# Optimization experiments

Measured on AMD Instinct MI355X. Metric: run time of the kernel, lower is better.

The kernel has to match this reference:

```python
import jax, jax.numpy as jnp
import numpy as np

H, U = 64, 64  # matrix-completion patch size; system size is (H*U)^2 = 4096^2


def svtC(X, tau):
    # Singular value thresholding: soft-threshold singular values by tau.
    u, s, vt = jnp.linalg.svd(X, full_matrices=False)
    return (u * jax.nn.relu(s - tau)) @ vt


def setup_inputs() -> dict:
    key = jax.random.key(0)
    ks = jax.random.split(key, 12)
    x = jax.random.normal(ks[0], (H, U), jnp.float32)
    L = jax.random.normal(ks[1], (H, U), jnp.float32)
    entries_mask = jax.random.randint(ks[2], (H, U), 0, 2).astype(bool)
    # D_tilda: symmetric PSD (HU, HU) smoothness operator so the system is well-conditioned
    M = jax.random.normal(ks[3], (H * U, H * U), jnp.float32)
    D_tilda = (M @ M.T) / jnp.float32(H * U)
    th_P = jax.random.normal(ks[4], (H, U), jnp.float32)
    v = jax.random.normal(ks[5], (), jnp.float32)
    coef_gamma = jax.random.uniform(ks[6], (), jnp.float32)
    neta = jax.random.uniform(ks[7], (), jnp.float32)
    lamda1 = jax.random.uniform(ks[8], (), jnp.float32)
    lamda2 = jax.random.uniform(ks[9], (), jnp.float32)
    rho = jax.random.uniform(ks[10], (), jnp.float32) + jnp.float32(0.1)
    S = jax.random.normal(ks[11], (H, H), jnp.float32) / np.float32(np.sqrt(H))
    return {"x": x, "L": L, "entries_mask": entries_mask, "D_tilda": D_tilda,
            "th_P": th_P, "v": v, "coef_gamma": coef_gamma, "neta": neta,
            "lamda1": lamda1, "lamda2": lamda2, "rho": rho, "S": S}


def reference(x, L, entries_mask, D_tilda, th_P, v, coef_gamma, neta,
              lamda1, lamda2, rho, S):
    tau = jax.nn.sigmoid(v) * coef_gamma
    # Q_tilda = diag(vec(mask)); S_tilda = kron(I_U, S^T S)
    q = entries_mask.astype(jnp.float32).reshape(-1)  # (HU,)
    StS = S.T @ S                                      # (H, H)
    S_tilda = jnp.kron(jnp.eye(U, dtype=jnp.float32), StS)  # (HU, HU)
    eye = jnp.eye(H * U, dtype=jnp.float32)
    A = jnp.diag(q) + lamda1 * D_tilda + lamda2 * S_tilda + rho * eye
    vec = rho * (L - th_P) + jnp.where(entries_mask, x, jnp.float32(0.0))
    # Original uses explicit dense inverse followed by matvec
    Xtmp = (jnp.linalg.inv(A) @ vec.reshape(-1)).reshape(H, U)
    Ltmp = svtC(Xtmp + th_P, tau)
    Ptmp = th_P + neta * (Xtmp - Ltmp)
    return Ltmp, Ptmp
```

## Files before the change

kernel.cpp:

```cpp
#include <hip/hip_runtime.h>
#include <cstddef>

#define HU    4096
#define NBLK  256
#define NTHR  512
#define MAXIT 100
#define TOL2  1e-7f

#define WS_STS  0
#define WS_DINV 4096
#define WS_R0   8192
#define WS_U0   12288
#define WS_W    16384
#define WS_BAR  24576
#define WS_FLG  (WS_BAR + 1024)
#define WS_END  (WS_FLG + 128)

typedef _Float16 half4v __attribute__((ext_vector_type(4)));

__device__ __forceinline__ float fastrcp(float x) {
  float r; asm("v_rcp_f32 %0, %1" : "=v"(r) : "v"(x)); return r;
}
__device__ __forceinline__ float fastsqrt(float x) {
  float r; asm("v_sqrt_f32 %0, %1" : "=v"(r) : "v"(x)); return r;
}
__device__ __forceinline__ float fastrsq(float x) {
  float r; asm("v_rsq_f32 %0, %1" : "=v"(r) : "v"(x)); return r;
}

__device__ __forceinline__ float waveReduce(float v) {
#pragma unroll
  for (int off = 32; off > 0; off >>= 1) v += __shfl_xor(v, off, 64);
  return v;
}

__device__ __forceinline__ float blockSum(float v, float* red) {
  v = waveReduce(v);
  if ((threadIdx.x & 63) == 0) red[threadIdx.x >> 6] = v;
  __syncthreads();
  float s = 0.f;
#pragma unroll
  for (int i = 0; i < 8; ++i) s += red[i];
  __syncthreads();
  return s;
}

__device__ __forceinline__ float gsync_dk(unsigned long long* slots,
                                          unsigned long long* flgq,
                                          unsigned gen, float* red) {
  __syncthreads();
  const int tid = threadIdx.x, lane = tid & 63, b = blockIdx.x;
  unsigned long long* arr = slots + (gen & 1) * 256;
  if (b == 0) {
    if (tid < 64) {
      if (lane == 0) {
        float s = 0.f;
#pragma unroll
        for (int i = 0; i < 8; ++i) s += red[i];
        __threadfence();
        __hip_atomic_store(&arr[0],
                           ((unsigned long long)gen << 32) | __float_as_uint(s),
                           __ATOMIC_RELEASE, __HIP_MEMORY_SCOPE_AGENT);
      }
      float dsum;
      for (;;) {
        const unsigned long long v0 = __hip_atomic_load(&arr[lane],
                                        __ATOMIC_RELAXED, __HIP_MEMORY_SCOPE_AGENT);
        const unsigned long long v1 = __hip_atomic_load(&arr[lane + 64],
                                        __ATOMIC_RELAXED, __HIP_MEMORY_SCOPE_AGENT);
        const unsigned long long v2 = __hip_atomic_load(&arr[lane + 128],
                                        __ATOMIC_RELAXED, __HIP_MEMORY_SCOPE_AGENT);
        const unsigned long long v3 = __hip_atomic_load(&arr[lane + 192],
                                        __ATOMIC_RELAXED, __HIP_MEMORY_SCOPE_AGENT);
        const bool ok = ((unsigned)(v0 >> 32) >= gen) && ((unsigned)(v1 >> 32) >= gen)
                     && ((unsigned)(v2 >> 32) >= gen) && ((unsigned)(v3 >> 32) >= gen);
        if (__all(ok)) {
          dsum = __uint_as_float((unsigned)v0) + __uint_as_float((unsigned)v1)
               + __uint_as_float((unsigned)v2) + __uint_as_float((unsigned)v3);
          break;
        }
        __builtin_amdgcn_s_sleep(1);
      }
      const float dk = waveReduce(dsum);
      __threadfence();
      if (lane < 8)
        __hip_atomic_store(&flgq[lane * 8],
                           ((unsigned long long)gen << 32) | __float_as_uint(dk),
                           __ATOMIC_RELEASE, __HIP_MEMORY_SCOPE_AGENT);
      if (lane == 0) red[0] = dk;
    }
  } else if (tid == 0) {
    float s = 0.f;
#pragma unroll
    for (int i = 0; i < 8; ++i) s += red[i];
    __threadfence();
    __hip_atomic_store(&arr[b],
                       ((unsigned long long)gen << 32) | __float_as_uint(s),
                       __ATOMIC_RELEASE, __HIP_MEMORY_SCOPE_AGENT);
    unsigned long long* fq = flgq + (b & 7) * 8;
    unsigned long long f;
    for (;;) {
      f = __hip_atomic_load(fq, __ATOMIC_RELAXED, __HIP_MEMORY_SCOPE_AGENT);
      if ((unsigned)(f >> 32) >= gen) break;
      __builtin_amdgcn_s_sleep(1);
    }
    __threadfence();
    red[0] = __uint_as_float((unsigned)f);
  }
  __syncthreads();
  const float dk = red[0];
  __syncthreads();
  return dk;
}

#define SWP 6
#define S_W 68

__device__ __forceinline__ float red16(float x) {
  int t;
  t = __builtin_amdgcn_update_dpp(0, __float_as_int(x), 0x128, 0xF, 0xF, false);
  x += __int_as_float(t);
  t = __builtin_amdgcn_update_dpp(0, __float_as_int(x), 0x124, 0xF, 0xF, false);
  x += __int_as_float(t);
  t = __builtin_amdgcn_update_dpp(0, __float_as_int(x), 0x122, 0xF, 0xF, false);
  x += __int_as_float(t);
  t = __builtin_amdgcn_update_dpp(0, __float_as_int(x), 0x121, 0xF, 0xF, false);
  x += __int_as_float(t);
  return x;
}

__device__ __forceinline__ int gf8mul(int a, int b) {
  int p = 0;
  if (b & 1) p ^= a;
  if (b & 2) p ^= (a << 1);
  if (b & 4) p ^= (a << 2);
  if (p & 16) p ^= 22;
  if (p & 8)  p ^= 11;
  return p;
}

__device__ __forceinline__ int sel8(const int c[8], int i) {
  int r = c[0];
  r = (i == 1) ? c[1] : r;
  r = (i == 2) ? c[2] : r;
  r = (i == 3) ? c[3] : r;
  r = (i == 4) ? c[4] : r;
  r = (i == 5) ? c[5] : r;
  r = (i == 6) ? c[6] : r;
  r = (i == 7) ? c[7] : r;
  return r;
}

__global__ void __launch_bounds__(NTHR, 1)
fused_kernel(const float* __restrict__ x_in, const float* __restrict__ L_in,
             const int* __restrict__ mask, const float* __restrict__ D,
             const float* __restrict__ thP, const float* __restrict__ S,
             const float* __restrict__ l1p, const float* __restrict__ l2p,
             const float* __restrict__ rhop, const float* __restrict__ vp,
             const float* __restrict__ cgp, const float* __restrict__ netap,
             float* __restrict__ ws, float* __restrict__ out)
{
  __shared__ __align__(16) float u_l[HU];
  __shared__ __align__(16) char pool[128 * 1024];
  __shared__ float red[8];
  __shared__ float g_s[64];
  unsigned long long* slots = (unsigned long long*)(ws + WS_BAR);
  unsigned long long* flgq  = (unsigned long long*)(ws + WS_FLG);
  const float* sts = ws + WS_STS;
  const float lam1 = *l1p, lam2 = *l2p, rho = *rhop;
  const int tid = threadIdx.x, b = blockIdx.x;
  const int wv = tid >> 6, lane = tid & 63;
  unsigned gen = 0;

  const int gtid = b * NTHR + tid;
  if (gtid < HU) {
    const int a = gtid >> 6, c = gtid & 63;
    float acc = 0.f, sdiag = 0.f;
    for (int h = 0; h < 64; ++h) {
      const float sa = S[h * 64 + a], sc = S[h * 64 + c];
      acc = fmaf(sa, sc, acc);
      sdiag = fmaf(sc, sc, sdiag);
    }
    ws[WS_STS + gtid] = acc;
    const float q = mask[gtid] ? 1.f : 0.f;
    const float diag = q + rho + lam1 * D[(size_t)gtid * (HU + 1)] + lam2 * sdiag;
    const float bb = rho * (L_in[gtid] - thP[gtid]) + (mask[gtid] ? x_in[gtid] : 0.f);
    const float di = 1.f / diag;
    ws[WS_DINV + gtid] = di;
    ws[WS_R0 + gtid] = bb;
    ws[WS_U0 + gtid] = bb * di;
  }

  {
    const float4* __restrict__ Dg = (const float4*)(D + (size_t)b * 16 * HU);
    half4v* __restrict__ Dh4 = (half4v*)pool;
    for (int o = tid; o < 16 * HU / 4; o += NTHR) {
      const float4 dv = Dg[o];
      half4v h;
      h[0] = (_Float16)dv.x; h[1] = (_Float16)dv.y;
      h[2] = (_Float16)dv.z; h[3] = (_Float16)dv.w;
      Dh4[o] = h;
    }
  }
  if (tid < 8) red[tid] = 0.f;
  gsync_dk(slots, flgq, ++gen, red);

  float r_reg[8], s_reg[8], dinv_reg[8];
  float acc0 = 0.f;
#pragma unroll
  for (int m = 0; m < 8; ++m) {
    const int i = tid + m * NTHR;
    const float rv = ws[WS_R0 + i], uv = ws[WS_U0 + i];
    r_reg[m] = rv; u_l[i] = uv; dinv_reg[m] = ws[WS_DINV + i];
    s_reg[m] = 0.f;
  }
  __syncthreads();
#pragma unroll
  for (int m = 0; m < 8; ++m) acc0 = fmaf(r_reg[m], u_l[tid + m * NTHR], acc0);
  const float gamma0 = blockSum(acc0, red);

  float p_arr[8], x_arr[8];
#pragma unroll
  for (int m = 0; m < 8; ++m) { p_arr[m] = 0.f; x_arr[m] = 0.f; }

  const int row0 = b * 16 + wv * 2;
  const int iq = row0 >> 6, j0 = row0 & 63;
  const float4* __restrict__ u4 = (const float4*)u_l;
  const float m0 = mask[row0] ? 1.f : 0.f;
  const float m1 = mask[row0 + 1] ? 1.f : 0.f;
  const float sts0 = sts[j0 * 64 + lane];
  const float sts1 = sts[j0 * 64 + 64 + lane];
  const float dex0 = D[(size_t)row0 * (HU + 1)];
  const float dex1 = D[(size_t)(row0 + 1) * (HU + 1)];
  const float diagf0 = m0 + rho + lam1 * (dex0 - (float)(_Float16)dex0);
  const float diagf1 = m1 + rho + lam1 * (dex1 - (float)(_Float16)dex1);
  const half4v* __restrict__ H0 = (const half4v*)((_Float16*)pool + (size_t)(wv * 2) * HU);
  const half4v* __restrict__ H1 = H0 + (HU / 4);

  float gamma = gamma0, gamma_prev = 1.f, alpha_prev = 1.f;
  for (int k = 0; k < MAXIT; ++k) {
    float* __restrict__ wbuf = ws + WS_W + (k & 1) * HU;
    {
      float acc_a = 0.f, acc_b = 0.f;
#pragma unroll
      for (int it = 0; it < 16; ++it) {
        const float4 uu = u4[it * 64 + lane];
        const half4v d0 = H0[it * 64 + lane];
        const half4v d1 = H1[it * 64 + lane];
        acc_a = fmaf((float)d0[0], uu.x, acc_a); acc_a = fmaf((float)d0[1], uu.y, acc_a);
        acc_a = fmaf((float)d0[2], uu.z, acc_a); acc_a = fmaf((float)d0[3], uu.w, acc_a);
        acc_b = fmaf((float)d1[0], uu.x, acc_b); acc_b = fmaf((float)d1[1], uu.y, acc_b);
        acc_b = fmaf((float)d1[2], uu.z, acc_b); acc_b = fmaf((float)d1[3], uu.w, acc_b);
      }
      const float us = u_l[iq * 64 + lane];
      float t0 = fmaf(lam1, acc_a, lam2 * (sts0 * us));
      float t1 = fmaf(lam1, acc_b, lam2 * (sts1 * us));
      t0 = waveReduce(t0);
      t1 = waveReduce(t1);
      const float u0v = u_l[row0], u1v = u_l[row0 + 1];
      const float w0 = t0 + diagf0 * u0v;
      const float w1 = t1 + diagf1 * u1v;
      if (lane == 0) {
        wbuf[row0] = w0;
        wbuf[row0 + 1] = w1;
        red[wv] = fmaf(w0, u0v, w1 * u1v);
      }
    }
    const float dk = gsync_dk(slots, flgq, ++gen, red);

    float wv_r[8];
#pragma unroll
    for (int m = 0; m < 8; ++m) wv_r[m] = wbuf[tid + m * NTHR];

    const float beta  = (k == 0) ? 0.f : gamma * fastrcp(gamma_prev);
    const float denom = (k == 0) ? dk  : (dk - beta * gamma * fastrcp(alpha_prev));
    const float alpha = gamma * fastrcp(denom);

    float acc = 0.f;
#pragma unroll
    for (int m = 0; m < 8; ++m) {
      const int i = tid + m * NTHR;
      const float uold = u_l[i];
      const float sv = (k == 0) ? wv_r[m] : fmaf(beta, s_reg[m], wv_r[m]);
      s_reg[m] = sv;
      const float rv = fmaf(-alpha, sv, r_reg[m]);
      r_reg[m] = rv;
      const float uv = rv * dinv_reg[m];
      u_l[i] = uv;
      acc = fmaf(rv, uv, acc);
      if (b == 0) {
        const float pk = (k == 0) ? uold : fmaf(beta, p_arr[m], uold);
        p_arr[m] = pk;
        x_arr[m] = fmaf(alpha, pk, x_arr[m]);
      }
    }
    const float gnext = blockSum(acc, red);

    gamma_prev = gamma;
    alpha_prev = alpha;
    gamma = gnext;
    if (!(gnext > TOL2 * gamma0)) break;
  }

  if (b != 0) return;

  float* Wl = (float*)pool;
  float* Yr = Wl + 64 * S_W;
  float* T1 = Yr + 64 * S_W;
  float* Wr = T1 + 64 * S_W;
  __syncthreads();

  float t0acc = 0.f;
#pragma unroll
  for (int mm = 0; mm < 8; ++mm) {
    const int i = tid + mm * NTHR;
    const int rr = i >> 6, cc = i & 63;
    const float y = x_arr[mm] + thP[i];
    Wl[cc * S_W + rr] = y;
    Yr[rr * S_W + cc] = y;
    t0acc = fmaf(y, y, t0acc);
  }
  const float T0 = blockSum(t0acc, red);
  const float thr = 1.6e-10f * T0 * T0;

  const int team = lane >> 4;
  const int sub  = lane & 15;

  for (int sweep = 0; sweep < SWP; ++sweep) {
    float offacc = 0.f;
    for (int mr = 0; mr < 9; ++mr) {
      int cols[8];
#pragma unroll
      for (int j = 0; j < 8; ++j)
        cols[j] = (mr == 8) ? (8 * wv + j) : (8 * j + (gf8mul(mr, j) ^ wv));
      for (int r = 0; r < 7; ++r) {
        const int pi = (team == 0) ? 7 : ((r + team) % 7);
        const int qi = (team == 0) ? (r % 7) : ((r + 7 - team) % 7);
        const int cp = sel8(cols, pi);
        const int cq = sel8(cols, qi);
        float4* wp = (float4*)(Wl + cp * S_W) + sub;
        float4* wq = (float4*)(Wl + cq * S_W) + sub;
        const float4 a = *wp, bb = *wq;
        float dpp = fmaf(a.x, a.x, fmaf(a.y, a.y, fmaf(a.z, a.z, a.w * a.w)));
        float dqq = fmaf(bb.x, bb.x, fmaf(bb.y, bb.y, fmaf(bb.z, bb.z, bb.w * bb.w)));
        float dpq = fmaf(a.x, bb.x, fmaf(a.y, bb.y, fmaf(a.z, bb.z, a.w * bb.w)));
        dpp = red16(dpp); dqq = red16(dqq); dpq = red16(dpq);
        offacc = fmaf(dpq, dpq, offacc);
        if (dpq * dpq > 1e-14f * dpp * dqq) {
          const float th = (dqq - dpp) * 0.5f * fastrcp(dpq);
          const float sg = (th >= 0.f) ? 1.f : -1.f;
          const float t  = sg * fastrcp(fabsf(th) + fastsqrt(fmaf(th, th, 1.f)));
          const float c1 = fastrsq(fmaf(t, t, 1.f));
          const float s1 = t * c1;
          float4 na, nb;
          na.x = c1 * a.x - s1 * bb.x;  nb.x = s1 * a.x + c1 * bb.x;
          na.y = c1 * a.y - s1 * bb.y;  nb.y = s1 * a.y + c1 * bb.y;
          na.z = c1 * a.z - s1 * bb.z;  nb.z = s1 * a.z + c1 * bb.z;
          na.w = c1 * a.w - s1 * bb.w;  nb.w = s1 * a.w + c1 * bb.w;
          *wp = na; *wq = nb;
        }
      }
      __syncthreads();
    }
    const float tot = blockSum(offacc, red);
    if (sweep >= 2 && tot < thr) break;
  }

  if (tid < 64) {
    const float4* wc = (const float4*)(Wl + tid * S_W);
    float nn = 0.f;
#pragma unroll
    for (int i2 = 0; i2 < 16; ++i2) {
      const float4 u = wc[i2];
      nn = fmaf(u.x, u.x, fmaf(u.y, u.y, fmaf(u.z, u.z, fmaf(u.w, u.w, nn))));
    }
    const float sv = sqrtf(nn);
    const float tau = (*cgp) / (1.f + expf(-(*vp)));
    g_s[tid] = (sv > tau) ? (sv - tau) / (sv * nn) : 0.f;
  }
  __syncthreads();

  const int j = tid & 63;
  const int ib = tid >> 6;

#pragma unroll
  for (int mm = 0; mm < 8; ++mm) {
    const int k = ib + 8 * mm;
    const float4* wcol = (const float4*)(Wl + k * S_W);
    float acc = 0.f;
#pragma unroll
    for (int i4 = 0; i4 < 16; ++i4) {
      const float4 wvv = wcol[i4];
      acc = fmaf(wvv.x, Yr[(4 * i4 + 0) * S_W + j], acc);
      acc = fmaf(wvv.y, Yr[(4 * i4 + 1) * S_W + j], acc);
      acc = fmaf(wvv.z, Yr[(4 * i4 + 2) * S_W + j], acc);
      acc = fmaf(wvv.w, Yr[(4 * i4 + 3) * S_W + j], acc);
    }
    T1[k * S_W + j] = acc;
  }
  for (int o = tid; o < 4096; o += 512) {
    const int i2 = o >> 6, kk = o & 63;
    Wr[i2 * S_W + kk] = Wl[kk * S_W + i2] * g_s[kk];
  }
  __syncthreads();

  const float neta = *netap;
#pragma unroll
  for (int mm = 0; mm < 8; ++mm) {
    const int i2 = ib + 8 * mm;
    const float4* wrow = (const float4*)(Wr + i2 * S_W);
    float acc = 0.f;
#pragma unroll
    for (int k4 = 0; k4 < 16; ++k4) {
      const float4 wvv = wrow[k4];
      acc = fmaf(wvv.x, T1[(4 * k4 + 0) * S_W + j], acc);
      acc = fmaf(wvv.y, T1[(4 * k4 + 1) * S_W + j], acc);
      acc = fmaf(wvv.z, T1[(4 * k4 + 2) * S_W + j], acc);
      acc = fmaf(wvv.w, T1[(4 * k4 + 3) * S_W + j], acc);
    }
    const int o = i2 * 64 + j;
    out[o] = acc;
    out[4096 + o] = thP[o] + neta * (x_arr[mm] - acc);
  }
}

extern "C" void kernel_launch(void* const* d_in, const int* in_sizes, int n_in,
                              void* d_out, int out_size, void* d_ws, size_t ws_size,
                              hipStream_t stream)
{
  const float* x_in  = (const float*)d_in[0];
  const float* L_in  = (const float*)d_in[1];
  const int*   mask  = (const int*)d_in[2];
  const float* D     = (const float*)d_in[3];
  const float* thP   = (const float*)d_in[4];
  const float* vp    = (const float*)d_in[5];
  const float* cgp   = (const float*)d_in[6];
  const float* netap = (const float*)d_in[7];
  const float* l1p   = (const float*)d_in[8];
  const float* l2p   = (const float*)d_in[9];
  const float* rhop  = (const float*)d_in[10];
  const float* S     = (const float*)d_in[11];
  float* ws  = (float*)d_ws;
  float* out = (float*)d_out;

  hipMemsetAsync(ws + WS_BAR, 0, (WS_END - WS_BAR) * sizeof(float), stream);

  void* args[] = { (void*)&x_in, (void*)&L_in, (void*)&mask, (void*)&D, (void*)&thP,
                   (void*)&S, (void*)&l1p, (void*)&l2p, (void*)&rhop,
                   (void*)&vp, (void*)&cgp, (void*)&netap, (void*)&ws, (void*)&out };
  hipLaunchCooperativeKernel((void*)fused_kernel, dim3(NBLK), dim3(NTHR),
                             args, 0, stream);
}
```

Baseline: 327.7 us.

## Split CG solve and SVT into separate kernels; keep Jacobi pairs in registers

Splits the fused cooperative kernel in two. A CG solve kernel writes the solution vector to workspace, and a single-block SVT kernel then reads it back. Inside the Jacobi sweep, the column pairs now stay in registers across the seven rounds and rotate between teams via wave shuffles, instead of being reloaded from and stored to LDS each round. This cuts LDS traffic and may lower register pressure in the CG kernel, at the cost of an extra kernel launch and a global round-trip for the solution.

Measured after the change: 364.5 us. +11.2%, slower.

```diff
diff --git a/kernel.cpp b/kernel.cpp
--- a/kernel.cpp
+++ b/kernel.cpp
@@ -12,7 +12,8 @@
 #define WS_R0   8192
 #define WS_U0   12288
 #define WS_W    16384
-#define WS_BAR  24576
+#define WS_X    24576
+#define WS_BAR  28672
 #define WS_FLG  (WS_BAR + 1024)
 #define WS_END  (WS_FLG + 128)
 
@@ -113,57 +114,16 @@
   return dk;
 }
 
-#define SWP 6
-#define S_W 68
-
-__device__ __forceinline__ float red16(float x) {
-  int t;
-  t = __builtin_amdgcn_update_dpp(0, __float_as_int(x), 0x128, 0xF, 0xF, false);
-  x += __int_as_float(t);
-  t = __builtin_amdgcn_update_dpp(0, __float_as_int(x), 0x124, 0xF, 0xF, false);
-  x += __int_as_float(t);
-  t = __builtin_amdgcn_update_dpp(0, __float_as_int(x), 0x122, 0xF, 0xF, false);
-  x += __int_as_float(t);
-  t = __builtin_amdgcn_update_dpp(0, __float_as_int(x), 0x121, 0xF, 0xF, false);
-  x += __int_as_float(t);
-  return x;
-}
-
-__device__ __forceinline__ int gf8mul(int a, int b) {
-  int p = 0;
-  if (b & 1) p ^= a;
-  if (b & 2) p ^= (a << 1);
-  if (b & 4) p ^= (a << 2);
-  if (p & 16) p ^= 22;
-  if (p & 8)  p ^= 11;
-  return p;
-}
-
-__device__ __forceinline__ int sel8(const int c[8], int i) {
-  int r = c[0];
-  r = (i == 1) ? c[1] : r;
-  r = (i == 2) ? c[2] : r;
-  r = (i == 3) ? c[3] : r;
-  r = (i == 4) ? c[4] : r;
-  r = (i == 5) ? c[5] : r;
-  r = (i == 6) ? c[6] : r;
-  r = (i == 7) ? c[7] : r;
-  return r;
-}
-
 __global__ void __launch_bounds__(NTHR, 1)
-fused_kernel(const float* __restrict__ x_in, const float* __restrict__ L_in,
-             const int* __restrict__ mask, const float* __restrict__ D,
-             const float* __restrict__ thP, const float* __restrict__ S,
-             const float* __restrict__ l1p, const float* __restrict__ l2p,
-             const float* __restrict__ rhop, const float* __restrict__ vp,
-             const float* __restrict__ cgp, const float* __restrict__ netap,
-             float* __restrict__ ws, float* __restrict__ out)
+cg_solve_kernel(const float* __restrict__ x_in, const float* __restrict__ L_in,
+                const int* __restrict__ mask, const float* __restrict__ D,
+                const float* __restrict__ thP, const float* __restrict__ S,
+                const float* __restrict__ l1p, const float* __restrict__ l2p,
+                const float* __restrict__ rhop, float* __restrict__ ws)
 {
   __shared__ __align__(16) float u_l[HU];
-  __shared__ __align__(16) char pool[128 * 1024];
+  __shared__ __align__(16) _Float16 Dh[16 * HU];
   __shared__ float red[8];
-  __shared__ float g_s[64];
   unsigned long long* slots = (unsigned long long*)(ws + WS_BAR);
   unsigned long long* flgq  = (unsigned long long*)(ws + WS_FLG);
   const float* sts = ws + WS_STS;
@@ -193,7 +153,7 @@
 
   {
     const float4* __restrict__ Dg = (const float4*)(D + (size_t)b * 16 * HU);
-    half4v* __restrict__ Dh4 = (half4v*)pool;
+    half4v* __restrict__ Dh4 = (half4v*)Dh;
     for (int o = tid; o < 16 * HU / 4; o += NTHR) {
       const float4 dv = Dg[o];
       half4v h;
@@ -234,7 +194,7 @@
   const float dex1 = D[(size_t)(row0 + 1) * (HU + 1)];
   const float diagf0 = m0 + rho + lam1 * (dex0 - (float)(_Float16)dex0);
   const float diagf1 = m1 + rho + lam1 * (dex1 - (float)(_Float16)dex1);
-  const half4v* __restrict__ H0 = (const half4v*)((_Float16*)pool + (size_t)(wv * 2) * HU);
+  const half4v* __restrict__ H0 = (const half4v*)(Dh + (size_t)(wv * 2) * HU);
   const half4v* __restrict__ H1 = H0 + (HU / 4);
 
   float gamma = gamma0, gamma_prev = 1.f, alpha_prev = 1.f;
@@ -302,20 +262,78 @@
     if (!(gnext > TOL2 * gamma0)) break;
   }
 
-  if (b != 0) return;
-
-  float* Wl = (float*)pool;
-  float* Yr = Wl + 64 * S_W;
-  float* T1 = Yr + 64 * S_W;
-  float* Wr = T1 + 64 * S_W;
-  __syncthreads();
+  if (b == 0) {
+#pragma unroll
+    for (int m = 0; m < 8; ++m) ws[WS_X + tid + m * NTHR] = x_arr[m];
+  }
+}
+
+#define SWP 6
+#define S_W 68
+
+__device__ __forceinline__ float red16(float x) {
+  int t;
+  t = __builtin_amdgcn_update_dpp(0, __float_as_int(x), 0x128, 0xF, 0xF, false);
+  x += __int_as_float(t);
+  t = __builtin_amdgcn_update_dpp(0, __float_as_int(x), 0x124, 0xF, 0xF, false);
+  x += __int_as_float(t);
+  t = __builtin_amdgcn_update_dpp(0, __float_as_int(x), 0x122, 0xF, 0xF, false);
+  x += __int_as_float(t);
+  t = __builtin_amdgcn_update_dpp(0, __float_as_int(x), 0x121, 0xF, 0xF, false);
+  x += __int_as_float(t);
+  return x;
+}
+
+__device__ __forceinline__ int gf8mul(int a, int b) {
+  int p = 0;
+  if (b & 1) p ^= a;
+  if (b & 2) p ^= (a << 1);
+  if (b & 4) p ^= (a << 2);
+  if (p & 16) p ^= 22;
+  if (p & 8)  p ^= 11;
+  return p;
+}
+
+__device__ __forceinline__ int sel8(const int c[8], int i) {
+  int r = c[0];
+  r = (i == 1) ? c[1] : r;
+  r = (i == 2) ? c[2] : r;
+  r = (i == 3) ? c[3] : r;
+  r = (i == 4) ? c[4] : r;
+  r = (i == 5) ? c[5] : r;
+  r = (i == 6) ? c[6] : r;
+  r = (i == 7) ? c[7] : r;
+  return r;
+}
+
+__device__ __forceinline__ float4 shfl4(const float4 v, int src) {
+  float4 r;
+  r.x = __shfl(v.x, src, 64);
+  r.y = __shfl(v.y, src, 64);
+  r.z = __shfl(v.z, src, 64);
+  r.w = __shfl(v.w, src, 64);
+  return r;
+}
+
+__global__ void __launch_bounds__(512)
+svt_kernel(const float* __restrict__ thP, const float* __restrict__ vp,
+           const float* __restrict__ cgp, const float* __restrict__ netap,
+           const float* __restrict__ ws, float* __restrict__ out)
+{
+  const float* xsol = ws + WS_X;
+  __shared__ __align__(16) float Wl[64 * S_W];
+  __shared__ __align__(16) float Yr[64 * S_W];
+  __shared__ __align__(16) float T1[64 * S_W];
+  __shared__ __align__(16) float Wr[64 * S_W];
+  __shared__ float g_s[64];
+  __shared__ float red[8];
+  const int tid = threadIdx.x;
+  const int wv = tid >> 6, lane = tid & 63;
 
   float t0acc = 0.f;
-#pragma unroll
-  for (int mm = 0; mm < 8; ++mm) {
-    const int i = tid + mm * NTHR;
-    const int rr = i >> 6, cc = i & 63;
-    const float y = x_arr[mm] + thP[i];
+  for (int o = tid; o < 4096; o += 512) {
+    const int rr = o >> 6, cc = o & 63;
+    const float y = xsol[o] + thP[o];
     Wl[cc * S_W + rr] = y;
     Yr[rr * S_W + cc] = y;
     t0acc = fmaf(y, y, t0acc);
@@ -333,14 +351,12 @@
 #pragma unroll
       for (int j = 0; j < 8; ++j)
         cols[j] = (mr == 8) ? (8 * wv + j) : (8 * j + (gf8mul(mr, j) ^ wv));
+      const int cp_col = sel8(cols, team);
+      const int cq_col = sel8(cols, 7 - team);
+      float4* wp = (float4*)(Wl + cp_col * S_W) + sub;
+      float4* wq = (float4*)(Wl + cq_col * S_W) + sub;
+      float4 a = *wp, bb = *wq;
       for (int r = 0; r < 7; ++r) {
-        const int pi = (team == 0) ? 7 : ((r + team) % 7);
-        const int qi = (team == 0) ? (r % 7) : ((r + 7 - team) % 7);
-        const int cp = sel8(cols, pi);
-        const int cq = sel8(cols, qi);
-        float4* wp = (float4*)(Wl + cp * S_W) + sub;
-        float4* wq = (float4*)(Wl + cq * S_W) + sub;
-        const float4 a = *wp, bb = *wq;
         float dpp = fmaf(a.x, a.x, fmaf(a.y, a.y, fmaf(a.z, a.z, a.w * a.w)));
         float dqq = fmaf(bb.x, bb.x, fmaf(bb.y, bb.y, fmaf(bb.z, bb.z, bb.w * bb.w)));
         float dpq = fmaf(a.x, bb.x, fmaf(a.y, bb.y, fmaf(a.z, bb.z, a.w * bb.w)));
@@ -357,9 +373,15 @@
           na.y = c1 * a.y - s1 * bb.y;  nb.y = s1 * a.y + c1 * bb.y;
           na.z = c1 * a.z - s1 * bb.z;  nb.z = s1 * a.z + c1 * bb.z;
           na.w = c1 * a.w - s1 * bb.w;  nb.w = s1 * a.w + c1 * bb.w;
-          *wp = na; *wq = nb;
+          a = na; bb = nb;
         }
-      }
+        const float4 paS = shfl4(a,  (lane + 16) & 63);
+        const float4 qaS = shfl4(bb, (lane + 48) & 63);
+        const float4 np = (team == 3) ? bb : ((team == 0) ? a : paS);
+        const float4 nq = (team == 0) ? paS : qaS;
+        a = np; bb = nq;
+      }
+      *wp = a; *wq = bb;
       __syncthreads();
     }
     const float tot = blockSum(offacc, red);
@@ -420,7 +442,7 @@
     }
     const int o = i2 * 64 + j;
     out[o] = acc;
-    out[4096 + o] = thP[o] + neta * (x_arr[mm] - acc);
+    out[4096 + o] = thP[o] + neta * (xsol[o] - acc);
   }
 }
 
@@ -446,8 +468,9 @@
   hipMemsetAsync(ws + WS_BAR, 0, (WS_END - WS_BAR) * sizeof(float), stream);
 
   void* args[] = { (void*)&x_in, (void*)&L_in, (void*)&mask, (void*)&D, (void*)&thP,
-                   (void*)&S, (void*)&l1p, (void*)&l2p, (void*)&rhop,
-                   (void*)&vp, (void*)&cgp, (void*)&netap, (void*)&ws, (void*)&out };
-  hipLaunchCooperativeKernel((void*)fused_kernel, dim3(NBLK), dim3(NTHR),
+                   (void*)&S, (void*)&l1p, (void*)&l2p, (void*)&rhop, (void*)&ws };
+  hipLaunchCooperativeKernel((void*)cg_solve_kernel, dim3(NBLK), dim3(NTHR),
                              args, 0, stream);
-}
+
+  svt_kernel<<<1, 512, 0, stream>>>(thP, vp, cgp, netap, ws, out);
+}
```
